# Optimization experiments

Measured on AMD Instinct MI355X. Metric: run time of the kernel, lower is better.

Reference implementation:

```python
import jax, jax.numpy as jnp
import numpy as np

N = 16384      # nodes (256 chess boards x 64 squares)
E = 393216     # edges (avg degree 24)
G = 256        # graphs
HID = 128
H = 4
C = 32         # head dim
L = 8          # 4 blocks x 2 GATv2Conv
NODE_DIM = 21
EDGE_DIM = 6


def setup_inputs() -> dict:
    key = jax.random.key(0)
    ks = jax.random.split(key, 12)
    x = jax.random.normal(ks[0], (N, NODE_DIM), jnp.float32)
    edge_index = jax.random.randint(ks[1], (2, E), 0, N, dtype=jnp.int32)
    edge_attr = jax.random.uniform(ks[2], (E, EDGE_DIM), dtype=jnp.float32)
    batch = jnp.sort(jax.random.randint(ks[3], (N,), 0, G, dtype=jnp.int32))

    def w(k, shape, fan_in):
        return jax.random.normal(k, shape, jnp.float32) * (1.0 / np.sqrt(fan_in))

    Win = w(ks[4], (NODE_DIM, HID), NODE_DIM)
    b_in = jnp.zeros((HID,), jnp.float32)
    Wl = w(ks[5], (L, HID, HID), HID)
    bl = jnp.zeros((L, HID), jnp.float32)
    Wr = w(ks[6], (L, HID, HID), HID)
    br = jnp.zeros((L, HID), jnp.float32)
    We = w(ks[7], (L, EDGE_DIM, HID), EDGE_DIM)
    att = w(ks[8], (L, H, C), C)
    bconv = jnp.zeros((L, HID), jnp.float32)
    gamma = jnp.ones((L, HID), jnp.float32)
    beta = jnp.zeros((L, HID), jnp.float32)
    W1 = w(ks[9], (HID, 64), HID)
    b1 = jnp.zeros((64,), jnp.float32)
    W2 = w(ks[10], (64, 3), 64)
    b2 = jnp.zeros((3,), jnp.float32)
    return dict(x=x, edge_index=edge_index, edge_attr=edge_attr, batch=batch,
                Win=Win, b_in=b_in, Wl=Wl, bl=bl, Wr=Wr, br=br, We=We, att=att,
                bconv=bconv, gamma=gamma, beta=beta, W1=W1, b1=b1, W2=W2, b2=b2)


def _gatv2(h, src, dst, ea, Wl, bl, Wr, br, We, att, bias):
    # PyG GATv2Conv: message j->i uses x_j from lin_l, x_i from lin_r
    xl = (h @ Wl + bl).reshape(N, H, C)
    xr = (h @ Wr + br).reshape(N, H, C)
    ee = (ea @ We).reshape(-1, H, C)
    m = jax.nn.leaky_relu(xl[src] + xr[dst] + ee, 0.2)   # [Ef, H, C]
    s = jnp.einsum('ehc,hc->eh', m, att)                 # [Ef, H]
    smax = jax.ops.segment_max(s, dst, num_segments=N)   # self-loops => no empty segs
    ex = jnp.exp(s - smax[dst])
    den = jax.ops.segment_sum(ex, dst, num_segments=N)
    alpha = ex / den[dst]                                # edge softmax per target node
    out = jax.ops.segment_sum(alpha[:, :, None] * xl[src], dst, num_segments=N)
    return out.reshape(N, HID) + bias


def _bn(x, g, b):
    mu = jnp.mean(x, axis=0)
    var = jnp.var(x, axis=0)
    return g * (x - mu) * jax.lax.rsqrt(var + 1e-5) + b


def reference(x, edge_index, edge_attr, batch, Win, b_in, Wl, bl, Wr, br, We, att,
              bconv, gamma, beta, W1, b1, W2, b2):
    src0, dst0 = edge_index[0], edge_index[1]
    # add self-loops with fill_value='mean' (per-target mean of incoming edge_attr)
    deg = jax.ops.segment_sum(jnp.ones((E,), jnp.float32), dst0, num_segments=N)
    loop_attr = jax.ops.segment_sum(edge_attr, dst0, num_segments=N) / jnp.maximum(deg, 1.0)[:, None]
    idx = jnp.arange(N, dtype=src0.dtype)
    src = jnp.concatenate([src0, idx])
    dst = jnp.concatenate([dst0, idx])
    ea = jnp.concatenate([edge_attr, loop_attr], axis=0)

    h = jax.nn.relu(x @ Win + b_in)
    for blk in range(4):
        res = h
        l = 2 * blk
        h = jax.nn.relu(_bn(_gatv2(h, src, dst, ea, Wl[l], bl[l], Wr[l], br[l], We[l], att[l], bconv[l]), gamma[l], beta[l]))
        l = 2 * blk + 1
        h = _bn(_gatv2(h, src, dst, ea, Wl[l], bl[l], Wr[l], br[l], We[l], att[l], bconv[l]), gamma[l], beta[l])
        h = jax.nn.relu(h + res)

    cnt = jnp.maximum(jax.ops.segment_sum(jnp.ones((N,), jnp.float32), batch, num_segments=G), 1.0)
    pooled = jax.ops.segment_sum(h, batch, num_segments=G) / cnt[:, None]
    logits = jax.nn.relu(pooled @ W1 + b1) @ W2 + b2
    return logits
```

## Files before the change

kernel.cpp:

```cpp
#include <hip/hip_runtime.h>
#include <math.h>

constexpr int N   = 16384;
constexpr int E   = 393216;
constexpr int EF  = E + N;
constexpr int G   = 256;
constexpr int HID = 128;

__device__ __forceinline__ float red16(float x) {
    union fi { float f; int i; };
    fi a, b;
    a.f = x;
    b.i = __builtin_amdgcn_mov_dpp(a.i, 0x121, 0xf, 0xf, false); a.f += b.f;
    b.i = __builtin_amdgcn_mov_dpp(a.i, 0x122, 0xf, 0xf, false); a.f += b.f;
    b.i = __builtin_amdgcn_mov_dpp(a.i, 0x124, 0xf, 0xf, false); a.f += b.f;
    b.i = __builtin_amdgcn_mov_dpp(a.i, 0x128, 0xf, 0xf, false); a.f += b.f;
    return a.f;
}

__global__ __launch_bounds__(256) void k_hist(const int* __restrict__ dst,
                                              int* __restrict__ cnt) {
    int e = blockIdx.x * 256 + threadIdx.x;
    if (e < E) atomicAdd(&cnt[dst[e]], 1);
}

__global__ __launch_bounds__(1024) void k_scan(const int* __restrict__ cnt,
                                               int* __restrict__ row_ptr) {
    __shared__ int lds[1024];
    int t = threadIdx.x;
    int local[16];
    int s = 0;
    int base = t * 16;
#pragma unroll
    for (int q = 0; q < 16; q++) { local[q] = cnt[base + q] + 1; s += local[q]; }
    lds[t] = s;
    __syncthreads();
    for (int off = 1; off < 1024; off <<= 1) {
        int v = (t >= off) ? lds[t - off] : 0;
        __syncthreads();
        lds[t] += v;
        __syncthreads();
    }
    int run = (t == 0) ? 0 : lds[t - 1];
    if (t == 0) row_ptr[0] = 0;
#pragma unroll
    for (int q = 0; q < 16; q++) { run += local[q]; row_ptr[base + q + 1] = run; }
}

__global__ __launch_bounds__(256) void k_scatter(const int* __restrict__ src,
                                                 const int* __restrict__ dst,
                                                 const int* __restrict__ row_ptr,
                                                 int* __restrict__ cnt,
                                                 const float* __restrict__ edge_attr,
                                                 int* __restrict__ csr_src,
                                                 float* __restrict__ csr_ea) {
    int e = blockIdx.x * 256 + threadIdx.x;
    if (e >= E) return;
    int d = dst[e];
    int pos = row_ptr[d] + atomicSub(&cnt[d], 1) - 1;
    csr_src[pos] = src[e];
    const float* s = edge_attr + (size_t)e * 6;
    float4 a = {s[0], s[1], s[2], s[3]};
    float4 b = {s[4], s[5], 0.0f, 0.0f};
    float4* dstp = (float4*)(csr_ea + (size_t)pos * 8);
    dstp[0] = a;
    dstp[1] = b;
}

__global__ __launch_bounds__(256) void k_loopattr2(const int* __restrict__ row_ptr,
                                                   int* __restrict__ csr_src,
                                                   float* __restrict__ csr_ea) {
    int i = blockIdx.x * 256 + threadIdx.x;
    if (i >= N) return;
    int e0 = row_ptr[i], e1 = row_ptr[i + 1] - 1;
    float4 sa = {0, 0, 0, 0};
    float sbx = 0.0f, sby = 0.0f;
    for (int e = e0; e < e1; e++) {
        const float4* p = (const float4*)(csr_ea + (size_t)e * 8);
        float4 a = p[0];
        float4 b = p[1];
        sa.x += a.x; sa.y += a.y; sa.z += a.z; sa.w += a.w;
        sbx += b.x; sby += b.y;
    }
    float inv = 1.0f / fmaxf((float)(e1 - e0), 1.0f);
    float4 oa = {sa.x * inv, sa.y * inv, sa.z * inv, sa.w * inv};
    float4 ob = {sbx * inv, sby * inv, 0.0f, 0.0f};
    float4* q = (float4*)(csr_ea + (size_t)e1 * 8);
    q[0] = oa;
    q[1] = ob;
    csr_src[e1] = i;
}

__global__ __launch_bounds__(128) void k_ingemm(const float* __restrict__ x,
                                                const float* __restrict__ Win,
                                                const float* __restrict__ b_in,
                                                float* __restrict__ h) {
    __shared__ float xs[21];
    int i = blockIdx.x;
    int c = threadIdx.x;
    if (c < 21) xs[c] = x[i * 21 + c];
    __syncthreads();
    float acc = b_in[c];
#pragma unroll
    for (int d = 0; d < 21; d++) acc += xs[d] * Win[d * HID + c];
    h[i * HID + c] = fmaxf(acc, 0.0f);
}

__global__ __launch_bounds__(256) void k_gemm_lr(const float* __restrict__ h,
                                                 const float* __restrict__ bns,
                                                 const float* __restrict__ gamma,
                                                 const float* __restrict__ beta,
                                                 float* __restrict__ res,
                                                 const float* __restrict__ Wl,
                                                 const float* __restrict__ bl,
                                                 const float* __restrict__ Wr,
                                                 const float* __restrict__ br,
                                                 float* __restrict__ XL,
                                                 float* __restrict__ XR) {
    __shared__ float hs[16][HID];
    __shared__ float sc[HID], sh[HID];
    int t = threadIdx.x;
    int r0 = blockIdx.x * 16;
    if (bns) {
        if (t < 128) {
            const float invN = 1.0f / (float)N;
            float mean = bns[t] * invN;
            float var  = bns[128 + t] * invN - mean * mean;
            float inv  = rsqrtf(var + 1e-5f);
            float s = gamma[t] * inv;
            sc[t] = s;
            sh[t] = beta[t] - mean * s;
        }
        __syncthreads();
    }
    {
        int row = t >> 4;
        int col = (t & 15) * 8;
        size_t base = (size_t)(r0 + row) * HID + col;
        const float4* src = (const float4*)&h[base];
        float4 a = src[0];
        float4 b = src[1];
        if (bns) {
            float4 s0 = *(const float4*)&sc[col];
            float4 s1 = *(const float4*)&sc[col + 4];
            float4 h0 = *(const float4*)&sh[col];
            float4 h1 = *(const float4*)&sh[col + 4];
            a.x = fmaf(a.x, s0.x, h0.x);
            a.y = fmaf(a.y, s0.y, h0.y);
            a.z = fmaf(a.z, s0.z, h0.z);
            a.w = fmaf(a.w, s0.w, h0.w);
            b.x = fmaf(b.x, s1.x, h1.x);
            b.y = fmaf(b.y, s1.y, h1.y);
            b.z = fmaf(b.z, s1.z, h1.z);
            b.w = fmaf(b.w, s1.w, h1.w);
            if (res) {
                const float4* rp = (const float4*)&res[base];
                float4 ra = rp[0];
                float4 rb = rp[1];
                a.x += ra.x; a.y += ra.y; a.z += ra.z; a.w += ra.w;
                b.x += rb.x; b.y += rb.y; b.z += rb.z; b.w += rb.w;
            }
            a.x = fmaxf(a.x, 0.0f); a.y = fmaxf(a.y, 0.0f);
            a.z = fmaxf(a.z, 0.0f); a.w = fmaxf(a.w, 0.0f);
            b.x = fmaxf(b.x, 0.0f); b.y = fmaxf(b.y, 0.0f);
            b.z = fmaxf(b.z, 0.0f); b.w = fmaxf(b.w, 0.0f);
            if (res) {
                float4* wp = (float4*)&res[base];
                wp[0] = a;
                wp[1] = b;
            }
        }
        float4* dst = (float4*)&hs[row][col];
        dst[0] = a;
        dst[1] = b;
    }
    __syncthreads();
    bool right = t >= 128;
    int cp = (t & 63) * 2;
    int rbase = ((t >> 6) & 1) * 8;
    const float* W    = right ? Wr : Wl;
    const float* bias = right ? br : bl;
    float* OUT        = right ? XR : XL;
    float b0 = bias[cp], b1 = bias[cp + 1];
    float acc0[8], acc1[8];
#pragma unroll
    for (int r = 0; r < 8; r++) { acc0[r] = b0; acc1[r] = b1; }
    for (int k = 0; k < HID; k += 4) {
        float4 h4[8];
#pragma unroll
        for (int r = 0; r < 8; r++) h4[r] = *(const float4*)&hs[rbase + r][k];
#pragma unroll
        for (int kk = 0; kk < 4; kk++) {
            float2 w = *(const float2*)&W[(size_t)(k + kk) * HID + cp];
#pragma unroll
            for (int r = 0; r < 8; r++) {
                float hv = ((const float*)&h4[r])[kk];
                acc0[r] = fmaf(hv, w.x, acc0[r]);
                acc1[r] = fmaf(hv, w.y, acc1[r]);
            }
        }
    }
#pragma unroll
    for (int r = 0; r < 8; r++) {
        float2 o = {acc0[r], acc1[r]};
        *(float2*)&OUT[(size_t)(r0 + rbase + r) * HID + cp] = o;
    }
}

__global__ __launch_bounds__(1024, 8) void k_edge(const int* __restrict__ row_ptr,
                                                  const int* __restrict__ csr_src,
                                                  const float* __restrict__ csr_ea,
                                                  const float* __restrict__ xl,
                                                  const float* __restrict__ xr,
                                                  const float* __restrict__ We_l,
                                                  const float* __restrict__ att_l,
                                                  float* __restrict__ gout,
                                                  float* __restrict__ bnsums) {
    __shared__ float red_lds[16][256];
    int w = threadIdx.x >> 6;
    int lane = threadIdx.x & 63;
    int hh = lane >> 4;
    int ss = lane & 15;
    int ch0 = hh * 32 + 2 * ss;
    int i = blockIdx.x * 16 + w;

    const float LOG2E = 1.44269504088896f;
    float a0 = att_l[ch0] * LOG2E, a1 = att_l[ch0 + 1] * LOG2E;
    float we0[6], we1[6];
#pragma unroll
    for (int d = 0; d < 6; d++) {
        float2 wv = *(const float2*)&We_l[d * HID + ch0];
        we0[d] = wv.x;
        we1[d] = wv.y;
    }

    float2 xr2 = *(const float2*)&xr[(size_t)i * HID + ch0];
    float rd = 0.0f, acc0 = 0.0f, acc1 = 0.0f;
    int e0 = __builtin_amdgcn_readfirstlane(row_ptr[i]);
    int e1 = __builtin_amdgcn_readfirstlane(row_ptr[i + 1]);

    auto ld_idx = [&](int e, int out[4]) {
#pragma unroll
        for (int k = 0; k < 4; k++) {
            int ec = e + k;
            ec = (ec < e1) ? ec : (e1 - 1);
            out[k] = __builtin_amdgcn_readfirstlane(csr_src[ec]);
        }
    };
    auto ld_xl = [&](const int idx[4], float2 out[4]) {
#pragma unroll
        for (int k = 0; k < 4; k++)
            out[k] = *(const float2*)&xl[(size_t)idx[k] * HID + ch0];
    };
    auto body = [&](int e, const float2 xlv[4]) {
#pragma unroll
        for (int k = 0; k < 4; k++) {
            int ee = e + k;
            int ec = (ee < e1) ? ee : (e1 - 1);
            const float4* ea4 = (const float4*)(csr_ea + (size_t)ec * 8);
            float4 eaA = ea4[0];
            float4 eaB = ea4[1];
            float u0 = eaA.x * we0[0], u1 = eaA.x * we1[0];
            u0 = fmaf(eaA.y, we0[1], u0); u1 = fmaf(eaA.y, we1[1], u1);
            u0 = fmaf(eaA.z, we0[2], u0); u1 = fmaf(eaA.z, we1[2], u1);
            u0 = fmaf(eaA.w, we0[3], u0); u1 = fmaf(eaA.w, we1[3], u1);
            u0 = fmaf(eaB.x, we0[4], u0); u1 = fmaf(eaB.x, we1[4], u1);
            u0 = fmaf(eaB.y, we0[5], u0); u1 = fmaf(eaB.y, we1[5], u1);
            float m0 = xlv[k].x + xr2.x + u0;
            float m1 = xlv[k].y + xr2.y + u1;
            m0 = fmaxf(m0, 0.2f * m0);
            m1 = fmaxf(m1, 0.2f * m1);
            float pv = m0 * a0;
            pv = fmaf(m1, a1, pv);
            pv = red16(pv);
            pv = (ee < e1) ? pv : -INFINITY;
            float ex = exp2f(pv);
            rd += ex;
            acc0 = fmaf(ex, xlv[k].x, acc0);
            acc1 = fmaf(ex, xlv[k].y, acc1);
        }
    };

    int iA[4], iB[4], iC[4];
    float2 x0[4], x1[4];
    ld_idx(e0, iA);
    ld_idx(e0 + 4, iB);
    ld_idx(e0 + 8, iC);
    ld_xl(iA, x0);
    for (int e = e0; e < e1; e += 8) {
        ld_xl(iB, x1);
        ld_idx(e + 12, iA);
        body(e, x0);
        ld_xl(iC, x0);
        ld_idx(e + 16, iC);
        if (e + 4 < e1) body(e + 4, x1);
#pragma unroll
        for (int k = 0; k < 4; k++) iB[k] = iA[k];
    }
    float inv = 1.0f / rd;
    float2 o = {acc0 * inv, acc1 * inv};
    *(float2*)&gout[(size_t)i * HID + ch0] = o;

    red_lds[w][ch0]           = o.x;
    red_lds[w][ch0 + 1]       = o.y;
    red_lds[w][128 + ch0]     = o.x * o.x;
    red_lds[w][128 + ch0 + 1] = o.y * o.y;
    __syncthreads();
    int t = threadIdx.x;
    if (t < 256) {
        float s = 0.0f;
#pragma unroll
        for (int q = 0; q < 16; q++) s += red_lds[q][t];
        atomicAdd(&bnsums[t], s);
    }
}

__global__ __launch_bounds__(128) void k_pool(const float* __restrict__ gout,
                                              const float* __restrict__ res,
                                              const float* __restrict__ bns,
                                              const float* __restrict__ gamma,
                                              const float* __restrict__ beta,
                                              const int* __restrict__ batch,
                                              const float* __restrict__ W1,
                                              const float* __restrict__ b1,
                                              const float* __restrict__ W2,
                                              const float* __restrict__ b2,
                                              float* __restrict__ out) {
    __shared__ float pooled[HID];
    __shared__ float hid[64];
    __shared__ int bounds[2];
    int g = blockIdx.x;
    int t = threadIdx.x;
    if (t < 2) {
        int target = g + t;
        int lo = 0, hi = N;
        while (lo < hi) {
            int mid = (lo + hi) >> 1;
            if (batch[mid] < target) lo = mid + 1; else hi = mid;
        }
        bounds[t] = lo;
    }
    const float invN = 1.0f / (float)N;
    float mean = bns[t] * invN;
    float var  = bns[128 + t] * invN - mean * mean;
    float scb  = gamma[t] * rsqrtf(var + 1e-5f);
    float shb  = beta[t] - mean * scb;
    __syncthreads();
    int s = bounds[0], e = bounds[1];
    float acc = 0.0f;
    for (int r = s; r < e; r++) {
        float v = fmaf(gout[(size_t)r * HID + t], scb, shb) + res[(size_t)r * HID + t];
        acc += fmaxf(v, 0.0f);
    }
    float cntf = fmaxf((float)(e - s), 1.0f);
    pooled[t] = acc / cntf;
    __syncthreads();
    if (t < 64) {
        float a = b1[t];
#pragma unroll 4
        for (int c = 0; c < HID; c++) a += pooled[c] * W1[c * 64 + t];
        hid[t] = fmaxf(a, 0.0f);
    }
    __syncthreads();
    if (t < 3) {
        float a = b2[t];
#pragma unroll
        for (int j = 0; j < 64; j++) a += hid[j] * W2[j * 3 + t];
        out[g * 3 + t] = a;
    }
}

extern "C" void kernel_launch(void* const* d_in, const int* in_sizes, int n_in,
                              void* d_out, int out_size, void* d_ws, size_t ws_size,
                              hipStream_t stream) {
    const float* x         = (const float*)d_in[0];
    const int*   edge_index= (const int*)d_in[1];
    const float* edge_attr = (const float*)d_in[2];
    const int*   batch     = (const int*)d_in[3];
    const float* Win       = (const float*)d_in[4];
    const float* b_in      = (const float*)d_in[5];
    const float* Wl        = (const float*)d_in[6];
    const float* bl        = (const float*)d_in[7];
    const float* Wr        = (const float*)d_in[8];
    const float* br        = (const float*)d_in[9];
    const float* We        = (const float*)d_in[10];
    const float* att       = (const float*)d_in[11];
    const float* gamma     = (const float*)d_in[13];
    const float* beta      = (const float*)d_in[14];
    const float* W1        = (const float*)d_in[15];
    const float* b1        = (const float*)d_in[16];
    const float* W2        = (const float*)d_in[17];
    const float* b2        = (const float*)d_in[18];
    float* out = (float*)d_out;

    const int* src0 = edge_index;
    const int* dst0 = edge_index + E;

    char* ws = (char*)d_ws;
    size_t off = 0;
    auto alloc = [&](size_t bytes) -> void* {
        void* p = ws + off;
        off += (bytes + 255) & ~(size_t)255;
        return p;
    };
    int*   cnt       = (int*)alloc((size_t)N * sizeof(int));
    float* bnsums    = (float*)alloc((size_t)8 * 256 * sizeof(float));
    int*   row_ptr   = (int*)alloc((size_t)(N + 1) * sizeof(int));
    int*   csr_src   = (int*)alloc((size_t)EF * sizeof(int));
    float* csr_ea    = (float*)alloc((size_t)EF * 8 * sizeof(float));
    float* H0        = (float*)alloc((size_t)N * HID * sizeof(float));
    float* XL        = (float*)alloc((size_t)N * HID * sizeof(float));
    float* XR        = (float*)alloc((size_t)N * HID * sizeof(float));
    float* GOUT      = (float*)alloc((size_t)N * HID * sizeof(float));

    size_t zbytes = (size_t)N * sizeof(int) + 8 * 256 * sizeof(float);
    hipMemsetAsync(cnt, 0, zbytes, stream);
    k_hist<<<(E + 255) / 256, 256, 0, stream>>>(dst0, cnt);
    k_scan<<<1, 1024, 0, stream>>>(cnt, row_ptr);
    k_scatter<<<(E + 255) / 256, 256, 0, stream>>>(src0, dst0, row_ptr, cnt,
                                                   edge_attr, csr_src, csr_ea);
    k_loopattr2<<<(N + 255) / 256, 256, 0, stream>>>(row_ptr, csr_src, csr_ea);
    k_ingemm<<<N, 128, 0, stream>>>(x, Win, b_in, H0);

    for (int l = 0; l < 8; l++) {
        bool odd = (l & 1) != 0;
        const float* hin;
        const float* bns_in = nullptr;
        const float* g_in = nullptr;
        const float* b_in2 = nullptr;
        float* res = nullptr;
        if (l == 0) {
            hin = H0;
        } else {
            hin = GOUT;
            bns_in = bnsums + (l - 1) * 256;
            g_in  = gamma + (size_t)(l - 1) * HID;
            b_in2 = beta  + (size_t)(l - 1) * HID;
            if (!odd) res = H0;
        }
        k_gemm_lr<<<N / 16, 256, 0, stream>>>(hin, bns_in, g_in, b_in2, res,
                                              Wl + (size_t)l * HID * HID, bl + l * HID,
                                              Wr + (size_t)l * HID * HID, br + l * HID,
                                              XL, XR);
        k_edge<<<N / 16, 1024, 0, stream>>>(row_ptr, csr_src, csr_ea,
                                            XL, XR,
                                            We + (size_t)l * 6 * HID,
                                            att + (size_t)l * HID, GOUT,
                                            bnsums + l * 256);
    }
    k_pool<<<G, 128, 0, stream>>>(GOUT, H0, bnsums + 7 * 256,
                                  gamma + 7 * HID, beta + 7 * HID,
                                  batch, W1, b1, W2, b2, out);
}
```

Baseline: 728.9 us.

## Sort nodes by degree for edge kernel and peel remainder loop

Adds a degree histogram, scan and scatter that build a node order sorted by descending in-degree, and the edge kernel maps each wave to a node via this order. Waves within a block then have similar degrees, which reduces intra-block imbalance and tail waiting at the block barrier. The main loop now handles only full groups of four edges without clamping or masking, and a separate tail handles the remainder. The cost is three small setup kernels, an extra indirection, and loss of locality in output writes and xr reads.

```diff
diff --git a/kernel.cpp b/kernel.cpp
--- a/kernel.cpp
+++ b/kernel.cpp
@@ -89,6 +89,42 @@
     q[0] = oa;
     q[1] = ob;
     csr_src[e1] = i;
+}
+
+__global__ __launch_bounds__(256) void k_deghist(const int* __restrict__ row_ptr,
+                                                 int* __restrict__ dbins) {
+    int i = blockIdx.x * 256 + threadIdx.x;
+    if (i >= N) return;
+    int d = row_ptr[i + 1] - row_ptr[i];
+    d = d > 255 ? 255 : d;
+    atomicAdd(&dbins[d], 1);
+}
+
+__global__ __launch_bounds__(256) void k_degscan(const int* __restrict__ dbins,
+                                                 int* __restrict__ dbase) {
+    __shared__ int lds[256];
+    int t = threadIdx.x;
+    int own = dbins[255 - t];
+    lds[t] = own;
+    __syncthreads();
+    for (int off = 1; off < 256; off <<= 1) {
+        int v = (t >= off) ? lds[t - off] : 0;
+        __syncthreads();
+        lds[t] += v;
+        __syncthreads();
+    }
+    dbase[255 - t] = lds[t] - own;
+}
+
+__global__ __launch_bounds__(256) void k_degscatter(const int* __restrict__ row_ptr,
+                                                    int* __restrict__ dbase,
+                                                    int* __restrict__ order) {
+    int i = blockIdx.x * 256 + threadIdx.x;
+    if (i >= N) return;
+    int d = row_ptr[i + 1] - row_ptr[i];
+    d = d > 255 ? 255 : d;
+    int pos = atomicAdd(&dbase[d], 1);
+    order[pos] = i;
 }
 
 __global__ __launch_bounds__(128) void k_ingemm(const float* __restrict__ x,
@@ -208,6 +244,7 @@
 }
 
 __global__ __launch_bounds__(1024, 8) void k_edge(const int* __restrict__ row_ptr,
+                                                  const int* __restrict__ order,
                                                   const int* __restrict__ csr_src,
                                                   const float* __restrict__ csr_ea,
                                                   const float* __restrict__ xl,
@@ -222,7 +259,7 @@
     int hh = lane >> 4;
     int ss = lane & 15;
     int ch0 = hh * 32 + 2 * ss;
-    int i = blockIdx.x * 16 + w;
+    int i = order[blockIdx.x * 16 + w];
 
     const float LOG2E = 1.44269504088896f;
     float a0 = att_l[ch0] * LOG2E, a1 = att_l[ch0 + 1] * LOG2E;
@@ -238,6 +275,9 @@
     float rd = 0.0f, acc0 = 0.0f, acc1 = 0.0f;
     int e0 = __builtin_amdgcn_readfirstlane(row_ptr[i]);
     int e1 = __builtin_amdgcn_readfirstlane(row_ptr[i + 1]);
+    int deg = e1 - e0;
+    int nfull = deg >> 2;
+    int efull = e0 + (nfull << 2);
 
     auto ld_idx = [&](int e, int out[4]) {
 #pragma unroll
@@ -252,12 +292,10 @@
         for (int k = 0; k < 4; k++)
             out[k] = *(const float2*)&xl[(size_t)idx[k] * HID + ch0];
     };
-    auto body = [&](int e, const float2 xlv[4]) {
+    auto bodyF = [&](int e, const float2 xlv[4]) {
 #pragma unroll
         for (int k = 0; k < 4; k++) {
-            int ee = e + k;
-            int ec = (ee < e1) ? ee : (e1 - 1);
-            const float4* ea4 = (const float4*)(csr_ea + (size_t)ec * 8);
+            const float4* ea4 = (const float4*)(csr_ea + (size_t)(e + k) * 8);
             float4 eaA = ea4[0];
             float4 eaB = ea4[1];
             float u0 = eaA.x * we0[0], u1 = eaA.x * we1[0];
@@ -273,7 +311,6 @@
             float pv = m0 * a0;
             pv = fmaf(m1, a1, pv);
             pv = red16(pv);
-            pv = (ee < e1) ? pv : -INFINITY;
             float ex = exp2f(pv);
             rd += ex;
             acc0 = fmaf(ex, xlv[k].x, acc0);
@@ -287,15 +324,48 @@
     ld_idx(e0 + 4, iB);
     ld_idx(e0 + 8, iC);
     ld_xl(iA, x0);
-    for (int e = e0; e < e1; e += 8) {
+    for (int e = e0; e < efull; e += 8) {
         ld_xl(iB, x1);
         ld_idx(e + 12, iA);
-        body(e, x0);
+        bodyF(e, x0);
         ld_xl(iC, x0);
         ld_idx(e + 16, iC);
-        if (e + 4 < e1) body(e + 4, x1);
+        if (e + 4 < efull) bodyF(e + 4, x1);
 #pragma unroll
         for (int k = 0; k < 4; k++) iB[k] = iA[k];
+    }
+    int rem = deg & 3;
+    if (rem) {
+        int it[4];
+        float2 xt[4];
+        ld_idx(efull, it);
+        ld_xl(it, xt);
+#pragma unroll
+        for (int k = 0; k < 4; k++) {
+            int ee = efull + k;
+            int ec = (ee < e1) ? ee : (e1 - 1);
+            const float4* ea4 = (const float4*)(csr_ea + (size_t)ec * 8);
+            float4 eaA = ea4[0];
+            float4 eaB = ea4[1];
+            float u0 = eaA.x * we0[0], u1 = eaA.x * we1[0];
+            u0 = fmaf(eaA.y, we0[1], u0); u1 = fmaf(eaA.y, we1[1], u1);
+            u0 = fmaf(eaA.z, we0[2], u0); u1 = fmaf(eaA.z, we1[2], u1);
+            u0 = fmaf(eaA.w, we0[3], u0); u1 = fmaf(eaA.w, we1[3], u1);
+            u0 = fmaf(eaB.x, we0[4], u0); u1 = fmaf(eaB.x, we1[4], u1);
+            u0 = fmaf(eaB.y, we0[5], u0); u1 = fmaf(eaB.y, we1[5], u1);
+            float m0 = xt[k].x + xr2.x + u0;
+            float m1 = xt[k].y + xr2.y + u1;
+            m0 = fmaxf(m0, 0.2f * m0);
+            m1 = fmaxf(m1, 0.2f * m1);
+            float pv = m0 * a0;
+            pv = fmaf(m1, a1, pv);
+            pv = red16(pv);
+            pv = (ee < e1) ? pv : -INFINITY;
+            float ex = exp2f(pv);
+            rd += ex;
+            acc0 = fmaf(ex, xt[k].x, acc0);
+            acc1 = fmaf(ex, xt[k].y, acc1);
+        }
     }
     float inv = 1.0f / rd;
     float2 o = {acc0 * inv, acc1 * inv};
@@ -405,6 +475,9 @@
     };
     int*   cnt       = (int*)alloc((size_t)N * sizeof(int));
     float* bnsums    = (float*)alloc((size_t)8 * 256 * sizeof(float));
+    int*   dbins     = (int*)alloc((size_t)256 * sizeof(int));
+    int*   dbase     = (int*)alloc((size_t)256 * sizeof(int));
+    int*   order     = (int*)alloc((size_t)N * sizeof(int));
     int*   row_ptr   = (int*)alloc((size_t)(N + 1) * sizeof(int));
     int*   csr_src   = (int*)alloc((size_t)EF * sizeof(int));
     float* csr_ea    = (float*)alloc((size_t)EF * 8 * sizeof(float));
@@ -413,13 +486,17 @@
     float* XR        = (float*)alloc((size_t)N * HID * sizeof(float));
     float* GOUT      = (float*)alloc((size_t)N * HID * sizeof(float));
 
-    size_t zbytes = (size_t)N * sizeof(int) + 8 * 256 * sizeof(float);
+    size_t zbytes = (size_t)N * sizeof(int) + 8 * 256 * sizeof(float)
+                  + 256 * sizeof(int);
     hipMemsetAsync(cnt, 0, zbytes, stream);
     k_hist<<<(E + 255) / 256, 256, 0, stream>>>(dst0, cnt);
     k_scan<<<1, 1024, 0, stream>>>(cnt, row_ptr);
     k_scatter<<<(E + 255) / 256, 256, 0, stream>>>(src0, dst0, row_ptr, cnt,
                                                    edge_attr, csr_src, csr_ea);
     k_loopattr2<<<(N + 255) / 256, 256, 0, stream>>>(row_ptr, csr_src, csr_ea);
+    k_deghist<<<(N + 255) / 256, 256, 0, stream>>>(row_ptr, dbins);
+    k_degscan<<<1, 256, 0, stream>>>(dbins, dbase);
+    k_degscatter<<<(N + 255) / 256, 256, 0, stream>>>(row_ptr, dbase, order);
     k_ingemm<<<N, 128, 0, stream>>>(x, Win, b_in, H0);
 
     for (int l = 0; l < 8; l++) {
@@ -442,7 +519,7 @@
                                               Wl + (size_t)l * HID * HID, bl + l * HID,
                                               Wr + (size_t)l * HID * HID, br + l * HID,
                                               XL, XR);
-        k_edge<<<N / 16, 1024, 0, stream>>>(row_ptr, csr_src, csr_ea,
+        k_edge<<<N / 16, 1024, 0, stream>>>(row_ptr, order, csr_src, csr_ea,
                                             XL, XR,
                                             We + (size_t)l * 6 * HID,
                                             att + (size_t)l * HID, GOUT,
```

Result: slower. 814.0 us (+11.7%).

## Split BN stats from edge kernel, shrink blocks, prefetch edge attrs in pipeline

Applied to the files above, without the earlier changes.

The edge aggregation kernel moves from 1024-thread blocks (16 nodes) to 256-thread blocks (4 nodes) and no longer reduces batch-norm statistics through LDS and a block barrier. A separate k_bnstats kernel now computes the per-channel sums. The main loop processes only full groups of four edges, software-pipelining edge-attribute loads alongside the index and xl gathers, with a masked tail for the remainder. This is meant to remove clamping and masking work from the hot loop and the barrier stall at the end of the kernel, at the cost of an extra launch and a re-read of GOUT for each layer.

```diff
diff --git a/kernel.cpp b/kernel.cpp
--- a/kernel.cpp
+++ b/kernel.cpp
@@ -207,22 +207,19 @@
     }
 }
 
-__global__ __launch_bounds__(1024, 8) void k_edge(const int* __restrict__ row_ptr,
-                                                  const int* __restrict__ csr_src,
-                                                  const float* __restrict__ csr_ea,
-                                                  const float* __restrict__ xl,
-                                                  const float* __restrict__ xr,
-                                                  const float* __restrict__ We_l,
-                                                  const float* __restrict__ att_l,
-                                                  float* __restrict__ gout,
-                                                  float* __restrict__ bnsums) {
-    __shared__ float red_lds[16][256];
-    int w = threadIdx.x >> 6;
+__global__ __launch_bounds__(256, 4) void k_edge(const int* __restrict__ row_ptr,
+                                                 const int* __restrict__ csr_src,
+                                                 const float* __restrict__ csr_ea,
+                                                 const float* __restrict__ xl,
+                                                 const float* __restrict__ xr,
+                                                 const float* __restrict__ We_l,
+                                                 const float* __restrict__ att_l,
+                                                 float* __restrict__ gout) {
+    int i = (blockIdx.x * 256 + threadIdx.x) >> 6;
     int lane = threadIdx.x & 63;
     int hh = lane >> 4;
     int ss = lane & 15;
     int ch0 = hh * 32 + 2 * ss;
-    int i = blockIdx.x * 16 + w;
 
     const float LOG2E = 1.44269504088896f;
     float a0 = att_l[ch0] * LOG2E, a1 = att_l[ch0 + 1] * LOG2E;
@@ -238,6 +235,9 @@
     float rd = 0.0f, acc0 = 0.0f, acc1 = 0.0f;
     int e0 = __builtin_amdgcn_readfirstlane(row_ptr[i]);
     int e1 = __builtin_amdgcn_readfirstlane(row_ptr[i + 1]);
+    int deg = e1 - e0;
+    int nfull = deg >> 2;
+    int efull = e0 + (nfull << 2);
 
     auto ld_idx = [&](int e, int out[4]) {
 #pragma unroll
@@ -252,22 +252,81 @@
         for (int k = 0; k < 4; k++)
             out[k] = *(const float2*)&xl[(size_t)idx[k] * HID + ch0];
     };
-    auto body = [&](int e, const float2 xlv[4]) {
+    auto ld_ea = [&](int e, float4 outA[4], float2 outB[4]) {
 #pragma unroll
         for (int k = 0; k < 4; k++) {
-            int ee = e + k;
+            const float* p = csr_ea + (size_t)(e + k) * 8;
+            outA[k] = *(const float4*)p;
+            outB[k] = *(const float2*)(p + 4);
+        }
+    };
+    auto bodyF = [&](const float2 xlv[4], const float4 eA[4], const float2 eB[4]) {
+#pragma unroll
+        for (int k = 0; k < 4; k++) {
+            float u0 = eA[k].x * we0[0], u1 = eA[k].x * we1[0];
+            u0 = fmaf(eA[k].y, we0[1], u0); u1 = fmaf(eA[k].y, we1[1], u1);
+            u0 = fmaf(eA[k].z, we0[2], u0); u1 = fmaf(eA[k].z, we1[2], u1);
+            u0 = fmaf(eA[k].w, we0[3], u0); u1 = fmaf(eA[k].w, we1[3], u1);
+            u0 = fmaf(eB[k].x, we0[4], u0); u1 = fmaf(eB[k].x, we1[4], u1);
+            u0 = fmaf(eB[k].y, we0[5], u0); u1 = fmaf(eB[k].y, we1[5], u1);
+            float m0 = xlv[k].x + xr2.x + u0;
+            float m1 = xlv[k].y + xr2.y + u1;
+            m0 = fmaxf(m0, 0.2f * m0);
+            m1 = fmaxf(m1, 0.2f * m1);
+            float pv = m0 * a0;
+            pv = fmaf(m1, a1, pv);
+            pv = red16(pv);
+            float ex = exp2f(pv);
+            rd += ex;
+            acc0 = fmaf(ex, xlv[k].x, acc0);
+            acc1 = fmaf(ex, xlv[k].y, acc1);
+        }
+    };
+
+    int iA[4], iB[4];
+    float2 x0[4], x1[4];
+    float4 A0[4], A1[4];
+    float2 B0[4], B1[4];
+    ld_idx(e0, iA);
+    ld_idx(e0 + 4, iB);
+    ld_xl(iA, x0);
+    ld_ea(e0, A0, B0);
+    int e = e0, nf = nfull;
+    while (nf >= 2) {
+        ld_idx(e + 8, iA);
+        ld_xl(iB, x1);
+        ld_ea(e + 4, A1, B1);
+        bodyF(x0, A0, B0);
+        ld_idx(e + 12, iB);
+        ld_xl(iA, x0);
+        ld_ea(e + 8, A0, B0);
+        bodyF(x1, A1, B1);
+        e += 8; nf -= 2;
+    }
+    if (nf == 1) {
+        bodyF(x0, A0, B0);
+    }
+    int rem = deg & 3;
+    if (rem) {
+        int it[4];
+        float2 xt[4];
+        ld_idx(efull, it);
+        ld_xl(it, xt);
+#pragma unroll
+        for (int k = 0; k < 4; k++) {
+            int ee = efull + k;
             int ec = (ee < e1) ? ee : (e1 - 1);
-            const float4* ea4 = (const float4*)(csr_ea + (size_t)ec * 8);
-            float4 eaA = ea4[0];
-            float4 eaB = ea4[1];
+            const float* p = csr_ea + (size_t)ec * 8;
+            float4 eaA = *(const float4*)p;
+            float2 eaB = *(const float2*)(p + 4);
             float u0 = eaA.x * we0[0], u1 = eaA.x * we1[0];
             u0 = fmaf(eaA.y, we0[1], u0); u1 = fmaf(eaA.y, we1[1], u1);
             u0 = fmaf(eaA.z, we0[2], u0); u1 = fmaf(eaA.z, we1[2], u1);
             u0 = fmaf(eaA.w, we0[3], u0); u1 = fmaf(eaA.w, we1[3], u1);
             u0 = fmaf(eaB.x, we0[4], u0); u1 = fmaf(eaB.x, we1[4], u1);
             u0 = fmaf(eaB.y, we0[5], u0); u1 = fmaf(eaB.y, we1[5], u1);
-            float m0 = xlv[k].x + xr2.x + u0;
-            float m1 = xlv[k].y + xr2.y + u1;
+            float m0 = xt[k].x + xr2.x + u0;
+            float m1 = xt[k].y + xr2.y + u1;
             m0 = fmaxf(m0, 0.2f * m0);
             m1 = fmaxf(m1, 0.2f * m1);
             float pv = m0 * a0;
@@ -276,42 +335,36 @@
             pv = (ee < e1) ? pv : -INFINITY;
             float ex = exp2f(pv);
             rd += ex;
-            acc0 = fmaf(ex, xlv[k].x, acc0);
-            acc1 = fmaf(ex, xlv[k].y, acc1);
-        }
-    };
-
-    int iA[4], iB[4], iC[4];
-    float2 x0[4], x1[4];
-    ld_idx(e0, iA);
-    ld_idx(e0 + 4, iB);
-    ld_idx(e0 + 8, iC);
-    ld_xl(iA, x0);
-    for (int e = e0; e < e1; e += 8) {
-        ld_xl(iB, x1);
-        ld_idx(e + 12, iA);
-        body(e, x0);
-        ld_xl(iC, x0);
-        ld_idx(e + 16, iC);
-        if (e + 4 < e1) body(e + 4, x1);
-#pragma unroll
-        for (int k = 0; k < 4; k++) iB[k] = iA[k];
+            acc0 = fmaf(ex, xt[k].x, acc0);
+            acc1 = fmaf(ex, xt[k].y, acc1);
+        }
     }
     float inv = 1.0f / rd;
     float2 o = {acc0 * inv, acc1 * inv};
     *(float2*)&gout[(size_t)i * HID + ch0] = o;
-
-    red_lds[w][ch0]           = o.x;
-    red_lds[w][ch0 + 1]       = o.y;
-    red_lds[w][128 + ch0]     = o.x * o.x;
-    red_lds[w][128 + ch0 + 1] = o.y * o.y;
-    __syncthreads();
+}
+
+__global__ __launch_bounds__(256) void k_bnstats(const float* __restrict__ v,
+                                                 float* __restrict__ sums) {
+    __shared__ float l_s[256], l_q[256];
     int t = threadIdx.x;
-    if (t < 256) {
-        float s = 0.0f;
-#pragma unroll
-        for (int q = 0; q < 16; q++) s += red_lds[q][t];
-        atomicAdd(&bnsums[t], s);
+    int c = t & 127;
+    int half = t >> 7;
+    int r = blockIdx.x * 64 + half;
+    float s = 0.0f, q = 0.0f;
+    for (int it = 0; it < 32; it++, r += 2) {
+        float val = v[(size_t)r * HID + c];
+        s += val;
+        q = fmaf(val, val, q);
+    }
+    l_s[t] = s; l_q[t] = q;
+    __syncthreads();
+    if (t < 128) {
+        s = l_s[t] + l_s[t + 128];
+        atomicAdd(&sums[c], s);
+    } else {
+        q = l_q[t] + l_q[t - 128];
+        atomicAdd(&sums[128 + c], q);
     }
 }
 
@@ -407,7 +460,7 @@
     float* bnsums    = (float*)alloc((size_t)8 * 256 * sizeof(float));
     int*   row_ptr   = (int*)alloc((size_t)(N + 1) * sizeof(int));
     int*   csr_src   = (int*)alloc((size_t)EF * sizeof(int));
-    float* csr_ea    = (float*)alloc((size_t)EF * 8 * sizeof(float));
+    float* csr_ea    = (float*)alloc((size_t)EF * 8 * sizeof(float) + 512);
     float* H0        = (float*)alloc((size_t)N * HID * sizeof(float));
     float* XL        = (float*)alloc((size_t)N * HID * sizeof(float));
     float* XR        = (float*)alloc((size_t)N * HID * sizeof(float));
@@ -442,11 +495,11 @@
                                               Wl + (size_t)l * HID * HID, bl + l * HID,
                                               Wr + (size_t)l * HID * HID, br + l * HID,
                                               XL, XR);
-        k_edge<<<N / 16, 1024, 0, stream>>>(row_ptr, csr_src, csr_ea,
-                                            XL, XR,
-                                            We + (size_t)l * 6 * HID,
-                                            att + (size_t)l * HID, GOUT,
-                                            bnsums + l * 256);
+        k_edge<<<N / 4, 256, 0, stream>>>(row_ptr, csr_src, csr_ea,
+                                          XL, XR,
+                                          We + (size_t)l * 6 * HID,
+                                          att + (size_t)l * HID, GOUT);
+        k_bnstats<<<256, 256, 0, stream>>>(GOUT, bnsums + l * 256);
     }
     k_pool<<<G, 128, 0, stream>>>(GOUT, H0, bnsums + 7 * 256,
                                   gamma + 7 * HID, beta + 7 * HID,
```

Result: no change. 721.5 us (-1.0%).
